# Kernel tuning notes

Measured on AMD Instinct MI355X. Metric: run time of the kernel, lower is better.

## Reference

```python
import jax, jax.numpy as jnp
import numpy as np

B, P, C = 128, 8732, 21          # batch, num_priors (SSD300), num_classes incl. background
TOP_K = 200
VAR0, VAR1 = 0.1, 0.2            # SSD prior variances
CONF_THRESH = 0.01
NMS_THRESH = 0.45


def setup_inputs() -> dict:
    key = jax.random.key(0)
    k1, k2, k3, k4 = jax.random.split(key, 4)
    loc_data = jax.random.normal(k1, (B, P, 4), jnp.float32)
    conf_data = jax.random.normal(k2, (B * P, C), jnp.float32)
    # priors: (cx, cy, w, h) in [0,1], positive widths/heights
    cxy = jax.random.uniform(k3, (P, 2), jnp.float32)
    wh = jax.random.uniform(k4, (P, 2), jnp.float32, minval=0.02, maxval=0.3)
    prior_data = jnp.concatenate([cxy, wh], axis=-1)
    return {"loc_data": loc_data, "conf_data": conf_data, "prior_data": prior_data}


def _decode(loc, priors):
    # loc: [B,P,4], priors: [P,4] (cx,cy,w,h) -> corner boxes [B,P,4]
    xy = priors[:, :2] + loc[..., :2] * VAR0 * priors[:, 2:]
    wh = priors[:, 2:] * jnp.exp(loc[..., 2:] * VAR1)
    return jnp.concatenate([xy - wh * 0.5, xy + wh * 0.5], axis=-1)


def _nms_single(boxes, scores, idxs):
    # boxes [P,4] corners, scores [P] (-1 where below conf_thresh), idxs [P] int class ids
    x1, y1, x2, y2 = boxes[:, 0], boxes[:, 1], boxes[:, 2], boxes[:, 3]
    areas = (x2 - x1) * (y2 - y1)

    def body(s, _):
        i = jnp.argmax(s)          # highest remaining score
        si = s[i]
        valid = si > 0.0
        bi = boxes[i]
        # IoU of bi against all boxes
        ix1 = jnp.maximum(bi[0], x1)
        iy1 = jnp.maximum(bi[1], y1)
        ix2 = jnp.minimum(bi[2], x2)
        iy2 = jnp.minimum(bi[3], y2)
        inter = jnp.maximum(ix2 - ix1, 0.0) * jnp.maximum(iy2 - iy1, 0.0)
        area_i = (bi[2] - bi[0]) * (bi[3] - bi[1])
        iou = inter / (area_i + areas - inter)
        # class-aware (batched) NMS: only suppress same-class boxes; also kills i itself (iou=1)
        suppress = (iou > NMS_THRESH) & (idxs == idxs[i])
        s_new = jnp.where(suppress, -1.0, s)
        row = jnp.where(
            valid,
            jnp.concatenate([bi, si[None], idxs[i].astype(jnp.float32)[None]]),
            jnp.zeros(6, dtype=boxes.dtype),
        )
        return s_new, row

    _, rows = jax.lax.scan(body, scores, None, length=TOP_K)
    return rows  # [TOP_K, 6] = (x1,y1,x2,y2,score,class)


def reference(loc_data, conf_data, prior_data):
    # softmax over classes, drop background, per-prior best fg class
    conf = jax.nn.softmax(conf_data, axis=-1)[:, 1:].reshape(B, P, C - 1)
    scores = conf.max(axis=-1)           # [B,P]
    cls = jnp.argmax(conf, axis=-1)      # [B,P] fg class id (0..C-2)
    boxes = _decode(loc_data, prior_data)  # [B,P,4]
    masked = jnp.where(scores > CONF_THRESH, scores, -1.0)
    return jax.vmap(_nms_single)(boxes, masked, cls)  # [B, TOP_K, 6]
```

## Files before the change

kernel.cpp:

```cpp
#include <hip/hip_runtime.h>


typedef unsigned long long u64;

#define BATCH 128
#define NPRIOR 8732
#define NCLS 21
#define TOPK 200
#define T 1024
#define TARGET 256
#define CAP 384
#define NBIN 4096
#define KW 6

__device__ __forceinline__ double exp_fast(double x) {
  const double LOG2E = 1.4426950408889634;
  const double LN2_HI = 6.93147180369123816490e-01;
  const double LN2_LO = 1.90821492927058770002e-10;
  double n = rint(x * LOG2E);
  double r = fma(-n, LN2_HI, x);
  r = fma(-n, LN2_LO, r);
  double p = 2.505210838544172e-08;
  p = fma(p, r, 2.755731922398589e-07);
  p = fma(p, r, 2.7557319223985893e-06);
  p = fma(p, r, 2.48015873015873e-05);
  p = fma(p, r, 1.984126984126984e-04);
  p = fma(p, r, 1.388888888888889e-03);
  p = fma(p, r, 8.333333333333333e-03);
  p = fma(p, r, 4.1666666666666664e-02);
  p = fma(p, r, 1.6666666666666666e-01);
  p = fma(p, r, 0.5);
  p = fma(p, r, 1.0);
  p = fma(p, r, 1.0);
  double scale = __longlong_as_double(((long long)(1023 + (int)n)) << 52);
  return p * scale;
}

__global__ __launch_bounds__(256) void prep_kernel(
    const float* __restrict__ conf, u64* __restrict__ keys) {
  __shared__ __align__(16) float srow[256 * NCLS];
  const int tid = threadIdx.x;
  const long long R0 = (long long)blockIdx.x * 256;
  const float4* src = (const float4*)(conf + R0 * NCLS);
  float4* dst = (float4*)srow;
  for (int k = tid; k < 1344; k += 256) dst[k] = src[k];
  __syncthreads();

  const float* row = srow + tid * NCLS;
  float m = row[0];
#pragma unroll
  for (int j = 1; j < NCLS; ++j) m = fmaxf(m, row[j]);
  float sum = __expf(row[0] - m);
  float bestr = row[1];
  float beste = __expf(row[1] - m);
  sum += beste;
  int bi = 1;
#pragma unroll
  for (int j = 2; j < NCLS; ++j) {
    float rv = row[j];
    float ej = __expf(rv - m);
    sum += ej;
    if (rv > bestr) { bestr = rv; bi = j; beste = ej; }
  }
  float score = __fdividef(beste, sum);

  const long long r = R0 + tid;
  const int p = (int)(r % NPRIOR);
  u64 key = 0ULL;
  if (score > 0.01f) {
    key = ((u64)__float_as_uint(score) << 32) |
          ((u64)(16383 - p) << 10) | (u64)(bi - 1);
  }
  keys[r] = key;
}

__device__ __forceinline__ void radix_cut(const int* hist, int tid, int tcap,
                                          int* wtot, int* cut) {
  if (tid == 0) cut[2] = 0;
  const int base = tid * 4;
  const int cs = hist[base] + hist[base + 1] + hist[base + 2] + hist[base + 3];
  const int lane = tid & 63;
  int suf = cs;
#pragma unroll
  for (int off = 1; off < 64; off <<= 1) {
    int v = __shfl_down(suf, off);
    if (lane + off < 64) suf += v;
  }
  if (lane == 0) wtot[tid >> 6] = suf;
  __syncthreads();
  if (tid < 16) {
    int v = wtot[tid];
    int s = v;
#pragma unroll
    for (int off = 1; off < 16; off <<= 1) {
      int o = __shfl_down(s, off);
      if (tid + off < 16) s += o;
    }
    if (tid == 0) wtot[16] = s;
    wtot[tid] = s - v;
  }
  __syncthreads();
  const int total = wtot[16];
  if (total > 0) {
    const int target = total < tcap ? total : tcap;
    const int S = suf + wtot[tid >> 6];
    const int Snext = S - cs;
    if (S >= target && Snext < target) {
      int acc = Snext;
      for (int bn = base + 3; bn >= base; --bn) {
        acc += hist[bn];
        if (acc >= target) {
          cut[0] = bn; cut[1] = acc - hist[bn]; cut[2] = acc;
          break;
        }
      }
    }
  }
  __syncthreads();
}

__global__ __launch_bounds__(T) void nms_kernel(
    const float* __restrict__ loc, const float* __restrict__ conf,
    const float* __restrict__ prior, const u64* __restrict__ keys,
    float* __restrict__ out) {
  __shared__ u64 Ks[NPRIOR];
  __shared__ int hist[NBIN];
  __shared__ u64 buf[CAP];
  __shared__ u64 ebuf[CAP];
  __shared__ u64 buf2[CAP];
  __shared__ float4 cbox[CAP];
  __shared__ float car[CAP];
  __shared__ int ccl[CAP];
  __shared__ u64 KILL[CAP * KW];
  __shared__ int wtot[17];
  __shared__ int cut1[3], cut2[3];
  __shared__ u64 Ash[KW], KFsh[KW], ACCsh[KW];
  __shared__ float4 abox[TOPK];
  __shared__ float aar[TOPK];
  __shared__ int acl[TOPK];
  __shared__ int sh_cnt, sh_nA;
  __shared__ u64 sh_ub;

  const int tid = threadIdx.x;
  const int b = blockIdx.x;
  const float* confb = conf + (long long)b * (NPRIOR * NCLS);
  const float4* loc4 = ((const float4*)loc) + (long long)b * NPRIOR;
  const float4* pr4 = (const float4*)prior;
  float* outb = out + (long long)b * (TOPK * 6);

  for (int i = tid; i < NPRIOR; i += T) Ks[i] = keys[(long long)b * NPRIOR + i];
  if (tid == 0) { sh_nA = 0; sh_ub = ~0ULL; }
  __syncthreads();

  while (true) {
    for (int i = tid; i < NBIN; i += T) hist[i] = 0;
    __syncthreads();
    const u64 ub = sh_ub;
    for (int i = tid; i < NPRIOR; i += T) {
      u64 k = Ks[i];
      if (k && k < ub) atomicAdd(&hist[(int)((k >> 46) & 0xFFF)], 1);
    }
    __syncthreads();
    radix_cut(hist, tid, TARGET, wtot, cut1);
    const int total = wtot[16];
    int M = cut1[2];
    if (M == 0) break;
    const int c1 = cut1[0];
    const int baseA = cut1[1];
    const bool need2 = (M > CAP);
    int c2 = 0;
    if (need2) {
      for (int i = tid; i < NBIN; i += T) hist[i] = 0;
      __syncthreads();
      for (int i = tid; i < NPRIOR; i += T) {
        u64 k = Ks[i];
        if (k && k < ub && (int)((k >> 46) & 0xFFF) == c1)
          atomicAdd(&hist[(int)((k >> 34) & 0xFFF)], 1);
      }
      __syncthreads();
      const int tcap2 = (total < TARGET ? total : TARGET) - baseA;
      radix_cut(hist, tid, tcap2, wtot, cut2);
      c2 = cut2[0];
      M = baseA + cut2[2];
      if (M > CAP) {
        int Md = M - hist[c2];
        if (Md > 0) { M = Md; c2 = c2 + 1; } else { M = CAP; }
      }
    }
    if (tid == 0) {
      sh_cnt = 0;
      sh_ub = need2 ? (((u64)c1 << 46) + ((u64)c2 << 34)) : ((u64)c1 << 46);
    }
    __syncthreads();
    for (int i = tid; i < NPRIOR; i += T) {
      u64 k = Ks[i];
      bool psel = false;
      if (k && k < ub) {
        int b1 = (int)((k >> 46) & 0xFFF);
        psel = need2 ? (b1 > c1 || (b1 == c1 && (int)((k >> 34) & 0xFFF) >= c2))
                     : (b1 >= c1);
      }
      u64 mask = __ballot(psel ? 1 : 0);
      if (mask) {
        int lane = tid & 63;
        int leader = __ffsll((unsigned long long)mask) - 1;
        int bpos = 0;
        if (lane == leader) bpos = atomicAdd(&sh_cnt, __popcll(mask));
        bpos = __shfl(bpos, leader);
        if (psel) {
          int pos = bpos + __popcll(mask & ((1ULL << lane) - 1ULL));
          if (pos < CAP) buf[pos] = k;
        }
      }
    }
    __syncthreads();
    int Mr = sh_cnt;
    if (Mr > CAP) Mr = CAP;
    if (Mr == 0) break;
    if (tid < Mr) {
      u64 ak = buf[tid];
      int cl = (int)(ak & 0x1FULL);
      int p = 16383 - (int)((ak >> 10) & 0x3FFFULL);
      const float* crow = confb + (long long)p * NCLS;
      float cr[NCLS];
#pragma unroll
      for (int j = 0; j < NCLS; ++j) cr[j] = crow[j];
      double m = (double)cr[0];
#pragma unroll
      for (int j = 1; j < NCLS; ++j) m = fmax(m, (double)cr[j]);
      double sum = 0.0, best = -1.0;
#pragma unroll
      for (int j = 0; j < NCLS; ++j) {
        double ej = exp_fast((double)cr[j] - m);
        sum += ej;
        if (j >= 1 && ej > best) best = ej;
      }
      double score = best / sum;
      u64 sb = (u64)__double_as_longlong(score);
      ebuf[tid] = ((sb >> 24) << 24) | ((u64)(16383 - p) << 10) | (u64)cl;
    }
    __syncthreads();
    if (tid < Mr) {
      u64 ka = ebuf[tid];
      int ra = 0;
      int i = 0;
      for (; i + 8 <= Mr; i += 8) {
        u64 k0 = ebuf[i], k1 = ebuf[i + 1], k2 = ebuf[i + 2], k3 = ebuf[i + 3];
        u64 k4 = ebuf[i + 4], k5 = ebuf[i + 5], k6 = ebuf[i + 6], k7 = ebuf[i + 7];
        ra += (int)(k0 > ka) + (int)(k1 > ka) + (int)(k2 > ka) + (int)(k3 > ka) +
              (int)(k4 > ka) + (int)(k5 > ka) + (int)(k6 > ka) + (int)(k7 > ka);
      }
      for (; i < Mr; ++i) ra += (int)(ebuf[i] > ka);
      buf2[ra] = ka;
    }
    if (tid < KW) { Ash[tid] = 0ULL; KFsh[tid] = 0ULL; }
    __syncthreads();
    const int nA0 = sh_nA;
    if (tid < Mr) {
      const int t = tid;
      u64 k = buf2[t];
      int cl = (int)(k & 0x1FULL);
      int p = 16383 - (int)((k >> 10) & 0x3FFFULL);
      float4 l = loc4[p];
      float4 pr = pr4[p];
      double cx = (double)pr.x + (double)l.x * 0.1 * (double)pr.z;
      double cy = (double)pr.y + (double)l.y * 0.1 * (double)pr.w;
      double w = (double)pr.z * exp_fast((double)l.z * 0.2);
      double h = (double)pr.w * exp_fast((double)l.w * 0.2);
      float x1 = (float)(cx - w * 0.5), y1 = (float)(cy - h * 0.5);
      float x2 = (float)(cx + w * 0.5), y2 = (float)(cy + h * 0.5);
      cbox[t] = make_float4(x1, y1, x2, y2);
      car[t] = (x2 - x1) * (y2 - y1);
      ccl[t] = cl;
    }
    __syncthreads();
    if (nA0 > 0 && tid < Mr) {
      const int t = tid;
      float4 my = cbox[t];
      float mar = car[t];
      int mcl = ccl[t];
      bool sup = false;
      for (int a = 0; a < nA0; ++a) {
        if (acl[a] == mcl) {
          float4 ab = abox[a];
          float ix1 = fmaxf(ab.x, my.x), iy1 = fmaxf(ab.y, my.y);
          float ix2 = fminf(ab.z, my.z), iy2 = fminf(ab.w, my.w);
          float inter = fmaxf(ix2 - ix1, 0.f) * fmaxf(iy2 - iy1, 0.f);
          if (inter > 0.45f * (aar[a] + mar - inter)) sup = true;
        }
      }
      if (sup) atomicOr(&Ash[t >> 6], 1ULL << (t & 63));
    }
    for (int idx = tid; idx < KW * 512; idx += T) {
      const int seg = idx >> 9;
      const int t = idx & 511;
      if (t < Mr) {
        const int i0 = seg * 64;
        int i1 = i0 + 64;
        if (i1 > Mr) i1 = Mr;
        u64 mm = 0ULL;
        if (i1 > t) {
          float4 my = cbox[t];
          float mar = car[t];
          int mcl = ccl[t];
          int is = (i0 > t + 1) ? i0 : (t + 1);
#pragma unroll 4
          for (int i = is; i < i1; ++i) {
            if (ccl[i] == mcl) {
              float4 cb = cbox[i];
              float ix1 = fmaxf(my.x, cb.x), iy1 = fmaxf(my.y, cb.y);
              float ix2 = fminf(my.z, cb.z), iy2 = fminf(my.w, cb.w);
              float inter = fmaxf(ix2 - ix1, 0.f) * fmaxf(iy2 - iy1, 0.f);
              if (inter > 0.45f * (mar + car[i] - inter))
                mm |= 1ULL << (i - i0);
            }
          }
        }
        KILL[t * KW + seg] = mm;
        if (mm) atomicOr(&KFsh[t >> 6], 1ULL << (t & 63));
      }
    }
    __syncthreads();
    if (tid < 64) {
      u64 A0, A1, A2, A3, A4, A5;
      {
        u64 v[KW];
#pragma unroll
        for (int w = 0; w < KW; ++w) {
          int rem = Mr - 64 * w;
          u64 vm = (rem >= 64) ? ~0ULL : (rem <= 0 ? 0ULL : ((1ULL << rem) - 1ULL));
          v[w] = vm & ~Ash[w];
        }
        A0 = v[0]; A1 = v[1]; A2 = v[2]; A3 = v[3]; A4 = v[4]; A5 = v[5];
      }
      u64 C0 = 0, C1 = 0, C2 = 0, C3 = 0, C4 = 0, C5 = 0;
      int nacc = nA0;
      bool full = false;
#define KILLUPD(cidx) do { const u64* kc = &KILL[(cidx) * KW];      \
      A0 &= ~kc[0]; A1 &= ~kc[1]; A2 &= ~kc[2];                     \
      A3 &= ~kc[3]; A4 &= ~kc[4]; A5 &= ~kc[5]; } while (0)
#define RESW(w, Aw, Cw) if (!full) {                                \
      const u64 KFw = KFsh[w];                                      \
      int lim = Mr - (w) * 64; if (lim > 64) lim = 64;              \
      for (int q = 0; q < lim; ++q) {                               \
        if ((Aw >> q) & 1ULL) {                                     \
          Cw |= 1ULL << q; ++nacc;                                  \
          if (nacc == TOPK) { full = true; break; }                 \
          if ((KFw >> q) & 1ULL) KILLUPD((w) * 64 + q);             \
        } } }
      RESW(0, A0, C0)
      RESW(1, A1, C1)
      RESW(2, A2, C2)
      RESW(3, A3, C3)
      RESW(4, A4, C4)
      RESW(5, A5, C5)
#undef RESW
#undef KILLUPD
      if (tid == 0) {
        ACCsh[0] = C0; ACCsh[1] = C1; ACCsh[2] = C2;
        ACCsh[3] = C3; ACCsh[4] = C4; ACCsh[5] = C5;
        sh_nA = nacc;
      }
    }
    __syncthreads();
    if (tid < Mr) {
      const int t = tid;
      const int w = t >> 6, q = t & 63;
      const u64 accw = ACCsh[w];
      if ((accw >> q) & 1ULL) {
        int rank = nA0;
#pragma unroll
        for (int w2 = 0; w2 < KW; ++w2)
          if (w2 < w) rank += __popcll(ACCsh[w2]);
        rank += __popcll(accw & ((q == 0) ? 0ULL : ((1ULL << q) - 1ULL)));
        float4 bx = cbox[t];
        float sc = (float)__longlong_as_double((long long)((buf2[t] >> 24) << 24));
        float* o = outb + rank * 6;
        o[0] = bx.x; o[1] = bx.y; o[2] = bx.z; o[3] = bx.w;
        o[4] = sc; o[5] = (float)ccl[t];
        abox[rank] = bx; aar[rank] = car[t]; acl[rank] = ccl[t];
      }
    }
    __syncthreads();
    if (sh_nA >= TOPK) break;
    if (total - Mr <= 0) break;
  }
  const int nAf = sh_nA;
  for (int i = nAf * 6 + tid; i < TOPK * 6; i += T) outb[i] = 0.0f;
}

extern "C" void kernel_launch(void* const* d_in, const int* in_sizes, int n_in,
                              void* d_out, int out_size, void* d_ws,
                              size_t ws_size, hipStream_t stream) {
  const float* loc = (const float*)d_in[0];
  const float* conf = (const float*)d_in[1];
  const float* prior = (const float*)d_in[2];
  float* out = (float*)d_out;

  u64* keys = (u64*)d_ws;

  const int nrows_blocks = (BATCH * NPRIOR) / 256;
  prep_kernel<<<nrows_blocks, 256, 0, stream>>>(conf, keys);
  nms_kernel<<<BATCH, T, 0, stream>>>(loc, conf, prior, keys, out);
}
```

Before: 208.7 us.

## Move first histogram and candidate selection into prep and a split select kernel

The prep kernel now builds per-batch 12-bit score histograms in global memory with atomics. A new select kernel, split four ways per batch, finds the radix cut and compacts candidate keys into a global buffer. The NMS kernel then starts from those precomputed candidates instead of copying all 8732 keys into shared memory and running the first histogram and compaction pass itself. The intent is to spread the selection work over more blocks and shrink the shared-memory footprint of the per-batch NMS kernel, at the cost of global atomics, a memset and an extra launch. Box decoding is also hoisted so loc and prior are loaded alongside the conf row.

```diff
diff --git a/kernel.cpp b/kernel.cpp
--- a/kernel.cpp
+++ b/kernel.cpp
@@ -12,6 +12,13 @@
 #define CAP 384
 #define NBIN 4096
 #define KW 6
+#define CSPL 4
+
+#define OFF_HIST 8941568ULL
+#define OFF_CAND 11038720ULL
+#define OFF_CNT 11431936ULL
+#define OFF_CUT 11432448ULL
+#define WS_NEED 11434496ULL
 
 __device__ __forceinline__ double exp_fast(double x) {
   const double LOG2E = 1.4426950408889634;
@@ -37,11 +44,12 @@
 }
 
 __global__ __launch_bounds__(256) void prep_kernel(
-    const float* __restrict__ conf, u64* __restrict__ keys) {
+    const float* __restrict__ conf, u64* __restrict__ keys,
+    int* __restrict__ histg) {
   __shared__ __align__(16) float srow[256 * NCLS];
   const int tid = threadIdx.x;
-  const long long R0 = (long long)blockIdx.x * 256;
-  const float4* src = (const float4*)(conf + R0 * NCLS);
+  const int R0 = blockIdx.x * 256;
+  const float4* src = (const float4*)(conf + (long long)R0 * NCLS);
   float4* dst = (float4*)srow;
   for (int k = tid; k < 1344; k += 256) dst[k] = src[k];
   __syncthreads();
@@ -64,12 +72,14 @@
   }
   float score = __fdividef(beste, sum);
 
-  const long long r = R0 + tid;
-  const int p = (int)(r % NPRIOR);
+  const int r = R0 + tid;
+  const int p = r % NPRIOR;
   u64 key = 0ULL;
   if (score > 0.01f) {
     key = ((u64)__float_as_uint(score) << 32) |
           ((u64)(16383 - p) << 10) | (u64)(bi - 1);
+    if (histg)
+      atomicAdd(&histg[(r / NPRIOR) * NBIN + (int)((key >> 46) & 0xFFF)], 1);
   }
   keys[r] = key;
 }
@@ -119,11 +129,55 @@
   __syncthreads();
 }
 
+__global__ __launch_bounds__(T) void select_kernel(
+    const u64* __restrict__ keys, const int* __restrict__ histg,
+    u64* __restrict__ cand, int* __restrict__ cnt, int4* __restrict__ cutinfo) {
+  __shared__ int hist[NBIN];
+  __shared__ int wtot[17];
+  __shared__ int cut[3];
+  const int tid = threadIdx.x;
+  const int b = blockIdx.x >> 2;
+  const int s = blockIdx.x & 3;
+  const int* hb = histg + b * NBIN;
+  for (int i = tid; i < NBIN; i += T) hist[i] = hb[i];
+  __syncthreads();
+  radix_cut(hist, tid, TARGET, wtot, cut);
+  const int total = wtot[16];
+  const int M = cut[2];
+  const int c1 = cut[0];
+  if (M == 0 || M > CAP) {
+    if (s == 0 && tid == 0) cutinfo[b] = make_int4(M > CAP ? 1 : 0, c1, total, M);
+    return;
+  }
+  if (s == 0 && tid == 0) cutinfo[b] = make_int4(0, c1, total, M);
+  const u64* kb = keys + (long long)b * NPRIOR;
+  const int chunk = (NPRIOR + CSPL - 1) / CSPL;
+  const int i0 = s * chunk;
+  int i1 = i0 + chunk;
+  if (i1 > NPRIOR) i1 = NPRIOR;
+  for (int i = i0 + tid; i < i1; i += T) {
+    u64 k = kb[i];
+    bool psel = (k != 0ULL) && ((int)((k >> 46) & 0xFFF) >= c1);
+    u64 mask = __ballot(psel ? 1 : 0);
+    if (mask) {
+      int lane = tid & 63;
+      int leader = __ffsll((unsigned long long)mask) - 1;
+      int bpos = 0;
+      if (lane == leader) bpos = atomicAdd(&cnt[b], __popcll(mask));
+      bpos = __shfl(bpos, leader);
+      if (psel) {
+        int pos = bpos + __popcll(mask & ((1ULL << lane) - 1ULL));
+        cand[(long long)b * CAP + pos] = k;
+      }
+    }
+  }
+}
+
 __global__ __launch_bounds__(T) void nms_kernel(
     const float* __restrict__ loc, const float* __restrict__ conf,
     const float* __restrict__ prior, const u64* __restrict__ keys,
+    const u64* __restrict__ cand, const int4* __restrict__ cutinfo,
     float* __restrict__ out) {
-  __shared__ u64 Ks[NPRIOR];
   __shared__ int hist[NBIN];
   __shared__ u64 buf[CAP];
   __shared__ u64 ebuf[CAP];
@@ -139,7 +193,6 @@
   __shared__ float aar[TOPK];
   __shared__ int acl[TOPK];
   __shared__ int sh_cnt, sh_nA;
-  __shared__ u64 sh_ub;
 
   const int tid = threadIdx.x;
   const int b = blockIdx.x;
@@ -147,244 +200,261 @@
   const float4* loc4 = ((const float4*)loc) + (long long)b * NPRIOR;
   const float4* pr4 = (const float4*)prior;
   float* outb = out + (long long)b * (TOPK * 6);
-
-  for (int i = tid; i < NPRIOR; i += T) Ks[i] = keys[(long long)b * NPRIOR + i];
-  if (tid == 0) { sh_nA = 0; sh_ub = ~0ULL; }
-  __syncthreads();
-
-  while (true) {
-    for (int i = tid; i < NBIN; i += T) hist[i] = 0;
-    __syncthreads();
-    const u64 ub = sh_ub;
-    for (int i = tid; i < NPRIOR; i += T) {
-      u64 k = Ks[i];
-      if (k && k < ub) atomicAdd(&hist[(int)((k >> 46) & 0xFFF)], 1);
-    }
-    __syncthreads();
-    radix_cut(hist, tid, TARGET, wtot, cut1);
-    const int total = wtot[16];
-    int M = cut1[2];
-    if (M == 0) break;
-    const int c1 = cut1[0];
-    const int baseA = cut1[1];
-    const bool need2 = (M > CAP);
-    int c2 = 0;
-    if (need2) {
-      for (int i = tid; i < NBIN; i += T) hist[i] = 0;
+  const u64* kb = keys + (long long)b * NPRIOR;
+
+  const int4 ci = cutinfo ? cutinfo[b] : make_int4(1, 0, 0, 0);
+  u64 ub = ~0ULL;
+  bool need_select = (ci.x != 0);
+  int Mr = 0, total = 0;
+  if (!need_select) {
+    total = ci.z;
+    Mr = ci.w;
+    if (tid < Mr) buf[tid] = cand[(long long)b * CAP + tid];
+    ub = (u64)ci.y << 46;
+  }
+  if (tid == 0) sh_nA = 0;
+
+  if (need_select || Mr > 0) {
+    while (true) {
+      if (need_select) {
+        for (int i = tid; i < NBIN; i += T) hist[i] = 0;
+        __syncthreads();
+        for (int i = tid; i < NPRIOR; i += T) {
+          u64 k = kb[i];
+          if (k && k < ub) atomicAdd(&hist[(int)((k >> 46) & 0xFFF)], 1);
+        }
+        __syncthreads();
+        radix_cut(hist, tid, TARGET, wtot, cut1);
+        total = wtot[16];
+        int M = cut1[2];
+        if (M == 0) break;
+        const int c1 = cut1[0];
+        const int baseA = cut1[1];
+        const bool need2 = (M > CAP);
+        int c2 = 0;
+        if (need2) {
+          for (int i = tid; i < NBIN; i += T) hist[i] = 0;
+          __syncthreads();
+          for (int i = tid; i < NPRIOR; i += T) {
+            u64 k = kb[i];
+            if (k && k < ub && (int)((k >> 46) & 0xFFF) == c1)
+              atomicAdd(&hist[(int)((k >> 34) & 0xFFF)], 1);
+          }
+          __syncthreads();
+          const int tcap2 = (total < TARGET ? total : TARGET) - baseA;
+          radix_cut(hist, tid, tcap2, wtot, cut2);
+          c2 = cut2[0];
+          M = baseA + cut2[2];
+          if (M > CAP) {
+            int Md = M - hist[c2];
+            if (Md > 0) { M = Md; c2 = c2 + 1; } else { M = CAP; }
+          }
+        }
+        if (tid == 0) sh_cnt = 0;
+        const u64 ubold = ub;
+        ub = need2 ? (((u64)c1 << 46) + ((u64)c2 << 34)) : ((u64)c1 << 46);
+        __syncthreads();
+        for (int i = tid; i < NPRIOR; i += T) {
+          u64 k = kb[i];
+          bool psel = false;
+          if (k && k < ubold) {
+            int b1 = (int)((k >> 46) & 0xFFF);
+            psel = need2
+                       ? (b1 > c1 || (b1 == c1 && (int)((k >> 34) & 0xFFF) >= c2))
+                       : (b1 >= c1);
+          }
+          u64 mask = __ballot(psel ? 1 : 0);
+          if (mask) {
+            int lane = tid & 63;
+            int leader = __ffsll((unsigned long long)mask) - 1;
+            int bpos = 0;
+            if (lane == leader) bpos = atomicAdd(&sh_cnt, __popcll(mask));
+            bpos = __shfl(bpos, leader);
+            if (psel) {
+              int pos = bpos + __popcll(mask & ((1ULL << lane) - 1ULL));
+              if (pos < CAP) buf[pos] = k;
+            }
+          }
+        }
+        __syncthreads();
+        Mr = sh_cnt;
+        if (Mr > CAP) Mr = CAP;
+        if (Mr == 0) break;
+      }
+
+      float4 lreg = make_float4(0.f, 0.f, 0.f, 0.f);
+      float4 preg = make_float4(0.f, 0.f, 0.f, 0.f);
+      int myp = 0, mycl = 0;
+      if (tid < Mr) {
+        u64 ak = buf[tid];
+        mycl = (int)(ak & 0x1FULL);
+        myp = 16383 - (int)((ak >> 10) & 0x3FFFULL);
+        lreg = loc4[myp];
+        preg = pr4[myp];
+        const float* crow = confb + (long long)myp * NCLS;
+        float cr[NCLS];
+#pragma unroll
+        for (int j = 0; j < NCLS; ++j) cr[j] = crow[j];
+        double m = (double)cr[0];
+#pragma unroll
+        for (int j = 1; j < NCLS; ++j) m = fmax(m, (double)cr[j]);
+        double sum = 0.0, best = -1.0;
+#pragma unroll
+        for (int j = 0; j < NCLS; ++j) {
+          double ej = exp_fast((double)cr[j] - m);
+          sum += ej;
+          if (j >= 1 && ej > best) best = ej;
+        }
+        double score = best / sum;
+        u64 sb = (u64)__double_as_longlong(score);
+        ebuf[tid] = ((sb >> 24) << 24) | ((u64)(16383 - myp) << 10) | (u64)mycl;
+      }
+      if (tid < KW) { Ash[tid] = 0ULL; KFsh[tid] = 0ULL; }
       __syncthreads();
-      for (int i = tid; i < NPRIOR; i += T) {
-        u64 k = Ks[i];
-        if (k && k < ub && (int)((k >> 46) & 0xFFF) == c1)
-          atomicAdd(&hist[(int)((k >> 34) & 0xFFF)], 1);
+      const int nA0 = sh_nA;
+
+      if (tid < Mr) {
+        u64 ka = ebuf[tid];
+        int ra = 0;
+        int i = 0;
+        for (; i + 8 <= Mr; i += 8) {
+          u64 k0 = ebuf[i], k1 = ebuf[i + 1], k2 = ebuf[i + 2], k3 = ebuf[i + 3];
+          u64 k4 = ebuf[i + 4], k5 = ebuf[i + 5], k6 = ebuf[i + 6],
+              k7 = ebuf[i + 7];
+          ra += (int)(k0 > ka) + (int)(k1 > ka) + (int)(k2 > ka) +
+                (int)(k3 > ka) + (int)(k4 > ka) + (int)(k5 > ka) +
+                (int)(k6 > ka) + (int)(k7 > ka);
+        }
+        for (; i < Mr; ++i) ra += (int)(ebuf[i] > ka);
+        buf2[ra] = ka;
+        double cx = (double)preg.x + (double)lreg.x * 0.1 * (double)preg.z;
+        double cy = (double)preg.y + (double)lreg.y * 0.1 * (double)preg.w;
+        double w = (double)preg.z * exp_fast((double)lreg.z * 0.2);
+        double h = (double)preg.w * exp_fast((double)lreg.w * 0.2);
+        float x1 = (float)(cx - w * 0.5), y1 = (float)(cy - h * 0.5);
+        float x2 = (float)(cx + w * 0.5), y2 = (float)(cy + h * 0.5);
+        cbox[ra] = make_float4(x1, y1, x2, y2);
+        car[ra] = (x2 - x1) * (y2 - y1);
+        ccl[ra] = mycl;
       }
       __syncthreads();
-      const int tcap2 = (total < TARGET ? total : TARGET) - baseA;
-      radix_cut(hist, tid, tcap2, wtot, cut2);
-      c2 = cut2[0];
-      M = baseA + cut2[2];
-      if (M > CAP) {
-        int Md = M - hist[c2];
-        if (Md > 0) { M = Md; c2 = c2 + 1; } else { M = CAP; }
-      }
-    }
-    if (tid == 0) {
-      sh_cnt = 0;
-      sh_ub = need2 ? (((u64)c1 << 46) + ((u64)c2 << 34)) : ((u64)c1 << 46);
-    }
-    __syncthreads();
-    for (int i = tid; i < NPRIOR; i += T) {
-      u64 k = Ks[i];
-      bool psel = false;
-      if (k && k < ub) {
-        int b1 = (int)((k >> 46) & 0xFFF);
-        psel = need2 ? (b1 > c1 || (b1 == c1 && (int)((k >> 34) & 0xFFF) >= c2))
-                     : (b1 >= c1);
-      }
-      u64 mask = __ballot(psel ? 1 : 0);
-      if (mask) {
-        int lane = tid & 63;
-        int leader = __ffsll((unsigned long long)mask) - 1;
-        int bpos = 0;
-        if (lane == leader) bpos = atomicAdd(&sh_cnt, __popcll(mask));
-        bpos = __shfl(bpos, leader);
-        if (psel) {
-          int pos = bpos + __popcll(mask & ((1ULL << lane) - 1ULL));
-          if (pos < CAP) buf[pos] = k;
-        }
-      }
-    }
-    __syncthreads();
-    int Mr = sh_cnt;
-    if (Mr > CAP) Mr = CAP;
-    if (Mr == 0) break;
-    if (tid < Mr) {
-      u64 ak = buf[tid];
-      int cl = (int)(ak & 0x1FULL);
-      int p = 16383 - (int)((ak >> 10) & 0x3FFFULL);
-      const float* crow = confb + (long long)p * NCLS;
-      float cr[NCLS];
-#pragma unroll
-      for (int j = 0; j < NCLS; ++j) cr[j] = crow[j];
-      double m = (double)cr[0];
-#pragma unroll
-      for (int j = 1; j < NCLS; ++j) m = fmax(m, (double)cr[j]);
-      double sum = 0.0, best = -1.0;
-#pragma unroll
-      for (int j = 0; j < NCLS; ++j) {
-        double ej = exp_fast((double)cr[j] - m);
-        sum += ej;
-        if (j >= 1 && ej > best) best = ej;
-      }
-      double score = best / sum;
-      u64 sb = (u64)__double_as_longlong(score);
-      ebuf[tid] = ((sb >> 24) << 24) | ((u64)(16383 - p) << 10) | (u64)cl;
-    }
-    __syncthreads();
-    if (tid < Mr) {
-      u64 ka = ebuf[tid];
-      int ra = 0;
-      int i = 0;
-      for (; i + 8 <= Mr; i += 8) {
-        u64 k0 = ebuf[i], k1 = ebuf[i + 1], k2 = ebuf[i + 2], k3 = ebuf[i + 3];
-        u64 k4 = ebuf[i + 4], k5 = ebuf[i + 5], k6 = ebuf[i + 6], k7 = ebuf[i + 7];
-        ra += (int)(k0 > ka) + (int)(k1 > ka) + (int)(k2 > ka) + (int)(k3 > ka) +
-              (int)(k4 > ka) + (int)(k5 > ka) + (int)(k6 > ka) + (int)(k7 > ka);
-      }
-      for (; i < Mr; ++i) ra += (int)(ebuf[i] > ka);
-      buf2[ra] = ka;
-    }
-    if (tid < KW) { Ash[tid] = 0ULL; KFsh[tid] = 0ULL; }
-    __syncthreads();
-    const int nA0 = sh_nA;
-    if (tid < Mr) {
-      const int t = tid;
-      u64 k = buf2[t];
-      int cl = (int)(k & 0x1FULL);
-      int p = 16383 - (int)((k >> 10) & 0x3FFFULL);
-      float4 l = loc4[p];
-      float4 pr = pr4[p];
-      double cx = (double)pr.x + (double)l.x * 0.1 * (double)pr.z;
-      double cy = (double)pr.y + (double)l.y * 0.1 * (double)pr.w;
-      double w = (double)pr.z * exp_fast((double)l.z * 0.2);
-      double h = (double)pr.w * exp_fast((double)l.w * 0.2);
-      float x1 = (float)(cx - w * 0.5), y1 = (float)(cy - h * 0.5);
-      float x2 = (float)(cx + w * 0.5), y2 = (float)(cy + h * 0.5);
-      cbox[t] = make_float4(x1, y1, x2, y2);
-      car[t] = (x2 - x1) * (y2 - y1);
-      ccl[t] = cl;
-    }
-    __syncthreads();
-    if (nA0 > 0 && tid < Mr) {
-      const int t = tid;
-      float4 my = cbox[t];
-      float mar = car[t];
-      int mcl = ccl[t];
-      bool sup = false;
-      for (int a = 0; a < nA0; ++a) {
-        if (acl[a] == mcl) {
-          float4 ab = abox[a];
-          float ix1 = fmaxf(ab.x, my.x), iy1 = fmaxf(ab.y, my.y);
-          float ix2 = fminf(ab.z, my.z), iy2 = fminf(ab.w, my.w);
-          float inter = fmaxf(ix2 - ix1, 0.f) * fmaxf(iy2 - iy1, 0.f);
-          if (inter > 0.45f * (aar[a] + mar - inter)) sup = true;
-        }
-      }
-      if (sup) atomicOr(&Ash[t >> 6], 1ULL << (t & 63));
-    }
-    for (int idx = tid; idx < KW * 512; idx += T) {
-      const int seg = idx >> 9;
-      const int t = idx & 511;
-      if (t < Mr) {
-        const int i0 = seg * 64;
-        int i1 = i0 + 64;
-        if (i1 > Mr) i1 = Mr;
-        u64 mm = 0ULL;
-        if (i1 > t) {
-          float4 my = cbox[t];
-          float mar = car[t];
-          int mcl = ccl[t];
-          int is = (i0 > t + 1) ? i0 : (t + 1);
+
+      if (nA0 > 0 && tid < Mr) {
+        const int t = tid;
+        float4 my = cbox[t];
+        float mar = car[t];
+        int mcl = ccl[t];
+        bool sup = false;
+        for (int a = 0; a < nA0; ++a) {
+          if (acl[a] == mcl) {
+            float4 ab = abox[a];
+            float ix1 = fmaxf(ab.x, my.x), iy1 = fmaxf(ab.y, my.y);
+            float ix2 = fminf(ab.z, my.z), iy2 = fminf(ab.w, my.w);
+            float inter = fmaxf(ix2 - ix1, 0.f) * fmaxf(iy2 - iy1, 0.f);
+            if (inter > 0.45f * (aar[a] + mar - inter)) sup = true;
+          }
+        }
+        if (sup) atomicOr(&Ash[t >> 6], 1ULL << (t & 63));
+      }
+      for (int idx = tid; idx < KW * 512; idx += T) {
+        const int seg = idx >> 9;
+        const int t = idx & 511;
+        if (t < Mr) {
+          const int i0 = seg * 64;
+          int i1 = i0 + 64;
+          if (i1 > Mr) i1 = Mr;
+          u64 mm = 0ULL;
+          if (i1 > t) {
+            float4 my = cbox[t];
+            float mar = car[t];
+            int mcl = ccl[t];
+            int is = (i0 > t + 1) ? i0 : (t + 1);
 #pragma unroll 4
-          for (int i = is; i < i1; ++i) {
-            if (ccl[i] == mcl) {
-              float4 cb = cbox[i];
-              float ix1 = fmaxf(my.x, cb.x), iy1 = fmaxf(my.y, cb.y);
-              float ix2 = fminf(my.z, cb.z), iy2 = fminf(my.w, cb.w);
-              float inter = fmaxf(ix2 - ix1, 0.f) * fmaxf(iy2 - iy1, 0.f);
-              if (inter > 0.45f * (mar + car[i] - inter))
-                mm |= 1ULL << (i - i0);
+            for (int i = is; i < i1; ++i) {
+              if (ccl[i] == mcl) {
+                float4 cb = cbox[i];
+                float ix1 = fmaxf(my.x, cb.x), iy1 = fmaxf(my.y, cb.y);
+                float ix2 = fminf(my.z, cb.z), iy2 = fminf(my.w, cb.w);
+                float inter = fmaxf(ix2 - ix1, 0.f) * fmaxf(iy2 - iy1, 0.f);
+                if (inter > 0.45f * (mar + car[i] - inter))
+                  mm |= 1ULL << (i - i0);
+              }
             }
           }
-        }
-        KILL[t * KW + seg] = mm;
-        if (mm) atomicOr(&KFsh[t >> 6], 1ULL << (t & 63));
-      }
-    }
-    __syncthreads();
-    if (tid < 64) {
-      u64 A0, A1, A2, A3, A4, A5;
-      {
-        u64 v[KW];
-#pragma unroll
-        for (int w = 0; w < KW; ++w) {
-          int rem = Mr - 64 * w;
-          u64 vm = (rem >= 64) ? ~0ULL : (rem <= 0 ? 0ULL : ((1ULL << rem) - 1ULL));
-          v[w] = vm & ~Ash[w];
-        }
-        A0 = v[0]; A1 = v[1]; A2 = v[2]; A3 = v[3]; A4 = v[4]; A5 = v[5];
-      }
-      u64 C0 = 0, C1 = 0, C2 = 0, C3 = 0, C4 = 0, C5 = 0;
-      int nacc = nA0;
-      bool full = false;
+          KILL[t * KW + seg] = mm;
+          if (mm) atomicOr(&KFsh[t >> 6], 1ULL << (t & 63));
+        }
+      }
+      __syncthreads();
+      if (tid < 64) {
+        u64 A0, A1, A2, A3, A4, A5;
+        {
+          u64 v[KW];
+#pragma unroll
+          for (int w = 0; w < KW; ++w) {
+            int rem = Mr - 64 * w;
+            u64 vm =
+                (rem >= 64) ? ~0ULL : (rem <= 0 ? 0ULL : ((1ULL << rem) - 1ULL));
+            v[w] = vm & ~Ash[w];
+          }
+          A0 = v[0]; A1 = v[1]; A2 = v[2]; A3 = v[3]; A4 = v[4]; A5 = v[5];
+        }
+        u64 C0 = 0, C1 = 0, C2 = 0, C3 = 0, C4 = 0, C5 = 0;
+        int nacc = nA0;
+        bool full = false;
 #define KILLUPD(cidx) do { const u64* kc = &KILL[(cidx) * KW];      \
-      A0 &= ~kc[0]; A1 &= ~kc[1]; A2 &= ~kc[2];                     \
-      A3 &= ~kc[3]; A4 &= ~kc[4]; A5 &= ~kc[5]; } while (0)
+        A0 &= ~kc[0]; A1 &= ~kc[1]; A2 &= ~kc[2];                   \
+        A3 &= ~kc[3]; A4 &= ~kc[4]; A5 &= ~kc[5]; } while (0)
 #define RESW(w, Aw, Cw) if (!full) {                                \
-      const u64 KFw = KFsh[w];                                      \
-      int lim = Mr - (w) * 64; if (lim > 64) lim = 64;              \
-      for (int q = 0; q < lim; ++q) {                               \
-        if ((Aw >> q) & 1ULL) {                                     \
-          Cw |= 1ULL << q; ++nacc;                                  \
-          if (nacc == TOPK) { full = true; break; }                 \
-          if ((KFw >> q) & 1ULL) KILLUPD((w) * 64 + q);             \
-        } } }
-      RESW(0, A0, C0)
-      RESW(1, A1, C1)
-      RESW(2, A2, C2)
-      RESW(3, A3, C3)
-      RESW(4, A4, C4)
-      RESW(5, A5, C5)
+        const u64 KFw = KFsh[w];                                    \
+        int lim = Mr - (w) * 64; if (lim > 64) lim = 64;            \
+        for (int q = 0; q < lim; ++q) {                             \
+          if ((Aw >> q) & 1ULL) {                                   \
+            Cw |= 1ULL << q; ++nacc;                                \
+            if (nacc == TOPK) { full = true; break; }               \
+            if ((KFw >> q) & 1ULL) KILLUPD((w) * 64 + q);           \
+          } } }
+        RESW(0, A0, C0)
+        RESW(1, A1, C1)
+        RESW(2, A2, C2)
+        RESW(3, A3, C3)
+        RESW(4, A4, C4)
+        RESW(5, A5, C5)
 #undef RESW
 #undef KILLUPD
-      if (tid == 0) {
-        ACCsh[0] = C0; ACCsh[1] = C1; ACCsh[2] = C2;
-        ACCsh[3] = C3; ACCsh[4] = C4; ACCsh[5] = C5;
-        sh_nA = nacc;
-      }
+        if (tid == 0) {
+          ACCsh[0] = C0; ACCsh[1] = C1; ACCsh[2] = C2;
+          ACCsh[3] = C3; ACCsh[4] = C4; ACCsh[5] = C5;
+          sh_nA = nacc;
+        }
+      }
+      __syncthreads();
+      if (tid < Mr) {
+        const int t = tid;
+        const int w = t >> 6, q = t & 63;
+        const u64 accw = ACCsh[w];
+        if ((accw >> q) & 1ULL) {
+          int rank = nA0;
+#pragma unroll
+          for (int w2 = 0; w2 < KW; ++w2)
+            if (w2 < w) rank += __popcll(ACCsh[w2]);
+          rank += __popcll(accw & ((q == 0) ? 0ULL : ((1ULL << q) - 1ULL)));
+          float4 bx = cbox[t];
+          float sc =
+              (float)__longlong_as_double((long long)((buf2[t] >> 24) << 24));
+          float* o = outb + rank * 6;
+          o[0] = bx.x; o[1] = bx.y; o[2] = bx.z; o[3] = bx.w;
+          o[4] = sc; o[5] = (float)ccl[t];
+          abox[rank] = bx; aar[rank] = car[t]; acl[rank] = ccl[t];
+        }
+      }
+      __syncthreads();
+      if (sh_nA >= TOPK) break;
+      if (total - Mr <= 0) break;
+      need_select = true;
     }
-    __syncthreads();
-    if (tid < Mr) {
-      const int t = tid;
-      const int w = t >> 6, q = t & 63;
-      const u64 accw = ACCsh[w];
-      if ((accw >> q) & 1ULL) {
-        int rank = nA0;
-#pragma unroll
-        for (int w2 = 0; w2 < KW; ++w2)
-          if (w2 < w) rank += __popcll(ACCsh[w2]);
-        rank += __popcll(accw & ((q == 0) ? 0ULL : ((1ULL << q) - 1ULL)));
-        float4 bx = cbox[t];
-        float sc = (float)__longlong_as_double((long long)((buf2[t] >> 24) << 24));
-        float* o = outb + rank * 6;
-        o[0] = bx.x; o[1] = bx.y; o[2] = bx.z; o[3] = bx.w;
-        o[4] = sc; o[5] = (float)ccl[t];
-        abox[rank] = bx; aar[rank] = car[t]; acl[rank] = ccl[t];
-      }
-    }
-    __syncthreads();
-    if (sh_nA >= TOPK) break;
-    if (total - Mr <= 0) break;
-  }
+  }
+  __syncthreads();
   const int nAf = sh_nA;
   for (int i = nAf * 6 + tid; i < TOPK * 6; i += T) outb[i] = 0.0f;
 }
@@ -397,9 +467,24 @@
   const float* prior = (const float*)d_in[2];
   float* out = (float*)d_out;
 
-  u64* keys = (u64*)d_ws;
-
+  char* ws = (char*)d_ws;
+  u64* keys = (u64*)ws;
   const int nrows_blocks = (BATCH * NPRIOR) / 256;
-  prep_kernel<<<nrows_blocks, 256, 0, stream>>>(conf, keys);
-  nms_kernel<<<BATCH, T, 0, stream>>>(loc, conf, prior, keys, out);
-}
+
+  if (ws_size >= WS_NEED) {
+    int* histg = (int*)(ws + OFF_HIST);
+    u64* cand = (u64*)(ws + OFF_CAND);
+    int* cnt = (int*)(ws + OFF_CNT);
+    int4* cutinfo = (int4*)(ws + OFF_CUT);
+    hipMemsetAsync(ws + OFF_HIST, 0, (size_t)(OFF_CUT - OFF_HIST), stream);
+    prep_kernel<<<nrows_blocks, 256, 0, stream>>>(conf, keys, histg);
+    select_kernel<<<BATCH * CSPL, T, 0, stream>>>(keys, histg, cand, cnt,
+                                                  cutinfo);
+    nms_kernel<<<BATCH, T, 0, stream>>>(loc, conf, prior, keys, cand, cutinfo,
+                                        out);
+  } else {
+    prep_kernel<<<nrows_blocks, 256, 0, stream>>>(conf, keys, nullptr);
+    nms_kernel<<<BATCH, T, 0, stream>>>(loc, conf, prior, keys, nullptr,
+                                        nullptr, out);
+  }
+}
```

New measurement: 303.9 us. 1.46x slower.

## Fuse softmax key prep into NMS kernel and hold keys in registers

Applied to the files above, without the earlier changes.

Removes the separate prep kernel. Each per-batch block now streams its own conf rows through LDS in chunks and computes the score keys itself, keeping them in registers (nine per thread) instead of a global workspace plus an LDS array. It also loads loc and prior earlier and merges the rank and box-decode phases, which drops one barrier. This saves a launch and the key write and read-back through global memory. The cost is that the softmax pass now runs on only 128 blocks with a barrier per chunk, so far fewer CUs pull the 94 MB of conf data and loads cannot overlap compute.

```diff
diff --git a/kernel.cpp b/kernel.cpp
--- a/kernel.cpp
+++ b/kernel.cpp
@@ -12,6 +12,7 @@
 #define CAP 384
 #define NBIN 4096
 #define KW 6
+#define NCHUNK 9
 
 __device__ __forceinline__ double exp_fast(double x) {
   const double LOG2E = 1.4426950408889634;
@@ -36,44 +37,6 @@
   return p * scale;
 }
 
-__global__ __launch_bounds__(256) void prep_kernel(
-    const float* __restrict__ conf, u64* __restrict__ keys) {
-  __shared__ __align__(16) float srow[256 * NCLS];
-  const int tid = threadIdx.x;
-  const long long R0 = (long long)blockIdx.x * 256;
-  const float4* src = (const float4*)(conf + R0 * NCLS);
-  float4* dst = (float4*)srow;
-  for (int k = tid; k < 1344; k += 256) dst[k] = src[k];
-  __syncthreads();
-
-  const float* row = srow + tid * NCLS;
-  float m = row[0];
-#pragma unroll
-  for (int j = 1; j < NCLS; ++j) m = fmaxf(m, row[j]);
-  float sum = __expf(row[0] - m);
-  float bestr = row[1];
-  float beste = __expf(row[1] - m);
-  sum += beste;
-  int bi = 1;
-#pragma unroll
-  for (int j = 2; j < NCLS; ++j) {
-    float rv = row[j];
-    float ej = __expf(rv - m);
-    sum += ej;
-    if (rv > bestr) { bestr = rv; bi = j; beste = ej; }
-  }
-  float score = __fdividef(beste, sum);
-
-  const long long r = R0 + tid;
-  const int p = (int)(r % NPRIOR);
-  u64 key = 0ULL;
-  if (score > 0.01f) {
-    key = ((u64)__float_as_uint(score) << 32) |
-          ((u64)(16383 - p) << 10) | (u64)(bi - 1);
-  }
-  keys[r] = key;
-}
-
 __device__ __forceinline__ void radix_cut(const int* hist, int tid, int tcap,
                                           int* wtot, int* cut) {
   if (tid == 0) cut[2] = 0;
@@ -119,11 +82,10 @@
   __syncthreads();
 }
 
-__global__ __launch_bounds__(T) void nms_kernel(
+__global__ __launch_bounds__(T) void detect_kernel(
     const float* __restrict__ loc, const float* __restrict__ conf,
-    const float* __restrict__ prior, const u64* __restrict__ keys,
-    float* __restrict__ out) {
-  __shared__ u64 Ks[NPRIOR];
+    const float* __restrict__ prior, float* __restrict__ out) {
+  __shared__ __align__(16) float srow[T * NCLS];
   __shared__ int hist[NBIN];
   __shared__ u64 buf[CAP];
   __shared__ u64 ebuf[CAP];
@@ -139,7 +101,6 @@
   __shared__ float aar[TOPK];
   __shared__ int acl[TOPK];
   __shared__ int sh_cnt, sh_nA;
-  __shared__ u64 sh_ub;
 
   const int tid = threadIdx.x;
   const int b = blockIdx.x;
@@ -148,21 +109,60 @@
   const float4* pr4 = (const float4*)prior;
   float* outb = out + (long long)b * (TOPK * 6);
 
-  for (int i = tid; i < NPRIOR; i += T) Ks[i] = keys[(long long)b * NPRIOR + i];
-  if (tid == 0) { sh_nA = 0; sh_ub = ~0ULL; }
-  __syncthreads();
-
+  u64 kreg[NCHUNK];
+#pragma unroll
+  for (int c = 0; c < NCHUNK; ++c) {
+    const int r0 = c * T;
+    const int nrows = (r0 + T <= NPRIOR) ? T : (NPRIOR - r0);
+    const int nf4 = (nrows * NCLS) >> 2;
+    const float4* src = (const float4*)(confb + (long long)r0 * NCLS);
+    float4* dst = (float4*)srow;
+    for (int k = tid; k < nf4; k += T) dst[k] = src[k];
+    __syncthreads();
+    u64 key = 0ULL;
+    if (tid < nrows) {
+      const float* row = srow + tid * NCLS;
+      float m = row[0];
+#pragma unroll
+      for (int j = 1; j < NCLS; ++j) m = fmaxf(m, row[j]);
+      float sum = __expf(row[0] - m);
+      float bestr = row[1];
+      float beste = __expf(row[1] - m);
+      sum += beste;
+      int bi = 1;
+#pragma unroll
+      for (int j = 2; j < NCLS; ++j) {
+        float rv = row[j];
+        float ej = __expf(rv - m);
+        sum += ej;
+        if (rv > bestr) { bestr = rv; bi = j; beste = ej; }
+      }
+      float score = __fdividef(beste, sum);
+      const int p = r0 + tid;
+      if (score > 0.01f) {
+        key = ((u64)__float_as_uint(score) << 32) |
+              ((u64)(16383 - p) << 10) | (u64)(bi - 1);
+      }
+    }
+    kreg[c] = key;
+    __syncthreads();
+  }
+
+  if (tid == 0) sh_nA = 0;
+
+  u64 ub = ~0ULL;
+  int Mr = 0, total = 0;
   while (true) {
     for (int i = tid; i < NBIN; i += T) hist[i] = 0;
     __syncthreads();
-    const u64 ub = sh_ub;
-    for (int i = tid; i < NPRIOR; i += T) {
-      u64 k = Ks[i];
+#pragma unroll
+    for (int c = 0; c < NCHUNK; ++c) {
+      u64 k = kreg[c];
       if (k && k < ub) atomicAdd(&hist[(int)((k >> 46) & 0xFFF)], 1);
     }
     __syncthreads();
     radix_cut(hist, tid, TARGET, wtot, cut1);
-    const int total = wtot[16];
+    total = wtot[16];
     int M = cut1[2];
     if (M == 0) break;
     const int c1 = cut1[0];
@@ -172,8 +172,9 @@
     if (need2) {
       for (int i = tid; i < NBIN; i += T) hist[i] = 0;
       __syncthreads();
-      for (int i = tid; i < NPRIOR; i += T) {
-        u64 k = Ks[i];
+#pragma unroll
+      for (int c = 0; c < NCHUNK; ++c) {
+        u64 k = kreg[c];
         if (k && k < ub && (int)((k >> 46) & 0xFFF) == c1)
           atomicAdd(&hist[(int)((k >> 34) & 0xFFF)], 1);
       }
@@ -187,15 +188,15 @@
         if (Md > 0) { M = Md; c2 = c2 + 1; } else { M = CAP; }
       }
     }
-    if (tid == 0) {
-      sh_cnt = 0;
-      sh_ub = need2 ? (((u64)c1 << 46) + ((u64)c2 << 34)) : ((u64)c1 << 46);
-    }
-    __syncthreads();
-    for (int i = tid; i < NPRIOR; i += T) {
-      u64 k = Ks[i];
+    if (tid == 0) sh_cnt = 0;
+    const u64 ubold = ub;
+    ub = need2 ? (((u64)c1 << 46) + ((u64)c2 << 34)) : ((u64)c1 << 46);
+    __syncthreads();
+#pragma unroll
+    for (int c = 0; c < NCHUNK; ++c) {
+      u64 k = kreg[c];
       bool psel = false;
-      if (k && k < ub) {
+      if (k && k < ubold) {
         int b1 = (int)((k >> 46) & 0xFFF);
         psel = need2 ? (b1 > c1 || (b1 == c1 && (int)((k >> 34) & 0xFFF) >= c2))
                      : (b1 >= c1);
@@ -214,14 +215,20 @@
       }
     }
     __syncthreads();
-    int Mr = sh_cnt;
+    Mr = sh_cnt;
     if (Mr > CAP) Mr = CAP;
     if (Mr == 0) break;
+
+    float4 lreg = make_float4(0.f, 0.f, 0.f, 0.f);
+    float4 preg = make_float4(0.f, 0.f, 0.f, 0.f);
+    int myp = 0, mycl = 0;
     if (tid < Mr) {
       u64 ak = buf[tid];
-      int cl = (int)(ak & 0x1FULL);
-      int p = 16383 - (int)((ak >> 10) & 0x3FFFULL);
-      const float* crow = confb + (long long)p * NCLS;
+      mycl = (int)(ak & 0x1FULL);
+      myp = 16383 - (int)((ak >> 10) & 0x3FFFULL);
+      lreg = loc4[myp];
+      preg = pr4[myp];
+      const float* crow = confb + (long long)myp * NCLS;
       float cr[NCLS];
 #pragma unroll
       for (int j = 0; j < NCLS; ++j) cr[j] = crow[j];
@@ -237,43 +244,38 @@
       }
       double score = best / sum;
       u64 sb = (u64)__double_as_longlong(score);
-      ebuf[tid] = ((sb >> 24) << 24) | ((u64)(16383 - p) << 10) | (u64)cl;
-    }
-    __syncthreads();
+      ebuf[tid] = ((sb >> 24) << 24) | ((u64)(16383 - myp) << 10) | (u64)mycl;
+    }
+    if (tid < KW) { Ash[tid] = 0ULL; KFsh[tid] = 0ULL; }
+    __syncthreads();
+    const int nA0 = sh_nA;
+
     if (tid < Mr) {
       u64 ka = ebuf[tid];
       int ra = 0;
       int i = 0;
       for (; i + 8 <= Mr; i += 8) {
         u64 k0 = ebuf[i], k1 = ebuf[i + 1], k2 = ebuf[i + 2], k3 = ebuf[i + 3];
-        u64 k4 = ebuf[i + 4], k5 = ebuf[i + 5], k6 = ebuf[i + 6], k7 = ebuf[i + 7];
-        ra += (int)(k0 > ka) + (int)(k1 > ka) + (int)(k2 > ka) + (int)(k3 > ka) +
-              (int)(k4 > ka) + (int)(k5 > ka) + (int)(k6 > ka) + (int)(k7 > ka);
+        u64 k4 = ebuf[i + 4], k5 = ebuf[i + 5], k6 = ebuf[i + 6],
+            k7 = ebuf[i + 7];
+        ra += (int)(k0 > ka) + (int)(k1 > ka) + (int)(k2 > ka) +
+              (int)(k3 > ka) + (int)(k4 > ka) + (int)(k5 > ka) +
+              (int)(k6 > ka) + (int)(k7 > ka);
       }
       for (; i < Mr; ++i) ra += (int)(ebuf[i] > ka);
       buf2[ra] = ka;
-    }
-    if (tid < KW) { Ash[tid] = 0ULL; KFsh[tid] = 0ULL; }
-    __syncthreads();
-    const int nA0 = sh_nA;
-    if (tid < Mr) {
-      const int t = tid;
-      u64 k = buf2[t];
-      int cl = (int)(k & 0x1FULL);
-      int p = 16383 - (int)((k >> 10) & 0x3FFFULL);
-      float4 l = loc4[p];
-      float4 pr = pr4[p];
-      double cx = (double)pr.x + (double)l.x * 0.1 * (double)pr.z;
-      double cy = (double)pr.y + (double)l.y * 0.1 * (double)pr.w;
-      double w = (double)pr.z * exp_fast((double)l.z * 0.2);
-      double h = (double)pr.w * exp_fast((double)l.w * 0.2);
+      double cx = (double)preg.x + (double)lreg.x * 0.1 * (double)preg.z;
+      double cy = (double)preg.y + (double)lreg.y * 0.1 * (double)preg.w;
+      double w = (double)preg.z * exp_fast((double)lreg.z * 0.2);
+      double h = (double)preg.w * exp_fast((double)lreg.w * 0.2);
       float x1 = (float)(cx - w * 0.5), y1 = (float)(cy - h * 0.5);
       float x2 = (float)(cx + w * 0.5), y2 = (float)(cy + h * 0.5);
-      cbox[t] = make_float4(x1, y1, x2, y2);
-      car[t] = (x2 - x1) * (y2 - y1);
-      ccl[t] = cl;
-    }
-    __syncthreads();
+      cbox[ra] = make_float4(x1, y1, x2, y2);
+      car[ra] = (x2 - x1) * (y2 - y1);
+      ccl[ra] = mycl;
+    }
+    __syncthreads();
+
     if (nA0 > 0 && tid < Mr) {
       const int t = tid;
       float4 my = cbox[t];
@@ -328,7 +330,8 @@
 #pragma unroll
         for (int w = 0; w < KW; ++w) {
           int rem = Mr - 64 * w;
-          u64 vm = (rem >= 64) ? ~0ULL : (rem <= 0 ? 0ULL : ((1ULL << rem) - 1ULL));
+          u64 vm =
+              (rem >= 64) ? ~0ULL : (rem <= 0 ? 0ULL : ((1ULL << rem) - 1ULL));
           v[w] = vm & ~Ash[w];
         }
         A0 = v[0]; A1 = v[1]; A2 = v[2]; A3 = v[3]; A4 = v[4]; A5 = v[5];
@@ -374,7 +377,8 @@
           if (w2 < w) rank += __popcll(ACCsh[w2]);
         rank += __popcll(accw & ((q == 0) ? 0ULL : ((1ULL << q) - 1ULL)));
         float4 bx = cbox[t];
-        float sc = (float)__longlong_as_double((long long)((buf2[t] >> 24) << 24));
+        float sc =
+            (float)__longlong_as_double((long long)((buf2[t] >> 24) << 24));
         float* o = outb + rank * 6;
         o[0] = bx.x; o[1] = bx.y; o[2] = bx.z; o[3] = bx.w;
         o[4] = sc; o[5] = (float)ccl[t];
@@ -385,6 +389,7 @@
     if (sh_nA >= TOPK) break;
     if (total - Mr <= 0) break;
   }
+  __syncthreads();
   const int nAf = sh_nA;
   for (int i = nAf * 6 + tid; i < TOPK * 6; i += T) outb[i] = 0.0f;
 }
@@ -396,10 +401,7 @@
   const float* conf = (const float*)d_in[1];
   const float* prior = (const float*)d_in[2];
   float* out = (float*)d_out;
-
-  u64* keys = (u64*)d_ws;
-
-  const int nrows_blocks = (BATCH * NPRIOR) / 256;
-  prep_kernel<<<nrows_blocks, 256, 0, stream>>>(conf, keys);
-  nms_kernel<<<BATCH, T, 0, stream>>>(loc, conf, prior, keys, out);
+  (void)d_ws; (void)ws_size;
+
+  detect_kernel<<<BATCH, T, 0, stream>>>(loc, conf, prior, out);
 }
```

New measurement: 228.7 us. 9.6% more time.
